# Optimization experiments

Hardware: AMD Instinct MI355X
Metric: run time of the kernel (lower is better)

Reference implementation:

```python
import jax, jax.numpy as jnp
import numpy as np
from jax import lax

V, E, H, K, B, T = 50000, 300, 512, 20, 64, 512  # vocab, embed, hidden, tags, batch, seqlen
HD = H // 2  # per-direction hidden


def setup_inputs() -> dict:
    key = jax.random.key(0)
    ks = jax.random.split(key, 12)
    s = 1.0 / np.sqrt(HD)
    inp = {
        "sentence": jax.random.randint(ks[0], (B, T), 0, V),
        "lengths": jax.random.randint(ks[1], (B,), T // 2, T + 1),
        "start_id": 18,
        "stop_id": 19,
        "embed_table": jax.random.normal(ks[2], (V, E), jnp.float32) * 0.9,
        "Wf_ih": jax.random.uniform(ks[3], (4 * HD, E), jnp.float32, -s, s),
        "Wf_hh": jax.random.uniform(ks[4], (4 * HD, HD), jnp.float32, -s, s),
        "bf": jax.random.uniform(ks[5], (4 * HD,), jnp.float32, -s, s),
        "Wb_ih": jax.random.uniform(ks[6], (4 * HD, E), jnp.float32, -s, s),
        "Wb_hh": jax.random.uniform(ks[7], (4 * HD, HD), jnp.float32, -s, s),
        "bb": jax.random.uniform(ks[8], (4 * HD,), jnp.float32, -s, s),
        "W_out": jax.random.uniform(ks[9], (K, H), jnp.float32, -s, s),
        "b_out": jax.random.uniform(ks[10], (K,), jnp.float32, -s, s),
    }
    trans = jax.random.normal(ks[11], (K, K), jnp.float32)
    trans = trans.at[18, :].set(-1000.0).at[:, 19].set(-1000.0)  # START row, STOP col
    inp["transitions"] = trans
    return inp


def _lstm(x, W_ih, W_hh, b):
    # x: [B, T, E] -> h: [B, T, HD], torch gate order i,f,g,o
    Bb = x.shape[0]
    Hd = W_hh.shape[1]
    h0 = jnp.zeros((Bb, Hd), x.dtype)

    def step(carry, xt):
        h, c = carry
        gates = xt @ W_ih.T + h @ W_hh.T + b
        i, f, g, o = jnp.split(gates, 4, axis=-1)
        c = jax.nn.sigmoid(f) * c + jax.nn.sigmoid(i) * jnp.tanh(g)
        h = jax.nn.sigmoid(o) * jnp.tanh(c)
        return (h, c), h

    _, hs = lax.scan(step, (h0, h0), x.transpose(1, 0, 2))
    return hs.transpose(1, 0, 2)


def _reverse_by_length(x, lengths):
    # reverse the valid prefix of each sequence, leaving padding in place
    t = jnp.arange(x.shape[1])[None, :]
    idx = jnp.where(t < lengths[:, None], lengths[:, None] - 1 - t, t)
    return jnp.take_along_axis(x, idx[:, :, None], axis=1)


def _emissions(sentence, lengths, embed_table, Wf_ih, Wf_hh, bf, Wb_ih, Wb_hh, bb, W_out, b_out):
    emb = embed_table[sentence]  # [B,T,E] (dropout is identity at inference)
    hf = _lstm(emb, Wf_ih, Wf_hh, bf)
    hb = _reverse_by_length(_lstm(_reverse_by_length(emb, lengths), Wb_ih, Wb_hh, bb), lengths)
    out = jnp.concatenate([hf, hb], axis=-1)  # [B,T,H]
    return out @ W_out.T + b_out  # [B,T,K]


def _viterbi(emis, lengths, transitions, stop_id):
    Bb, Tt, Kk = emis.shape
    delta0 = jnp.zeros((Bb, Kk), emis.dtype)  # faithful: init_vvars is all zeros
    valid = (jnp.arange(Tt)[None, :] < lengths[:, None]).T  # [T,B]
    ident = jnp.arange(Kk, dtype=jnp.int32)[None, :]

    def step(delta, inputs):
        emit_t, v = inputs  # [B,K], [B]
        scores = delta[:, None, :] + transitions[None, :, :]  # [B, next, prev]
        bp = jnp.argmax(scores, axis=-1).astype(jnp.int32)
        new_delta = jnp.max(scores, axis=-1) + emit_t
        delta = jnp.where(v[:, None], new_delta, delta)
        bp = jnp.where(v[:, None], bp, ident)  # pass-through at padded steps
        return delta, bp

    delta, bps = lax.scan(step, delta0, (emis.transpose(1, 0, 2), valid))
    terminal = delta + transitions[stop_id][None, :]
    best_last = jnp.argmax(terminal, axis=-1).astype(jnp.int32)  # [B]
    scores = jnp.max(terminal, axis=-1)  # [B]

    def backtrace(tag, bp_t):
        prev = jnp.take_along_axis(bp_t, tag[:, None], axis=1)[:, 0]
        return prev, prev

    _, prevs = lax.scan(backtrace, best_last, bps, reverse=True)  # [T,B]
    paths = jnp.concatenate([prevs, best_last[None, :]], axis=0).T  # [B,T+1], path[0]=START-step tag
    return scores, paths


def reference(sentence, lengths, start_id, stop_id, embed_table, Wf_ih, Wf_hh, bf,
              Wb_ih, Wb_hh, bb, W_out, b_out, transitions):
    emis = _emissions(sentence, lengths, embed_table, Wf_ih, Wf_hh, bf, Wb_ih, Wb_hh, bb, W_out, b_out)
    scores, paths = _viterbi(emis, lengths, transitions, stop_id)
    return scores, paths
```

## Files before the change

kernel.cpp:

```cpp
#include <hip/hip_runtime.h>
#include <math.h>

#define TT 512
#define BB 64
#define EE 300
#define HD 256
#define KK 20
#define NG 1024
#define RGC 8
#define RPBF 8
#define DPG 16
#define HS 260
#define LDSF (RPBF * HS)
#define LDS_FLOATS (2 * LDSF)
#define HXS 2048

__device__ __forceinline__ unsigned long long ldg_llc_u64(const unsigned long long* p) {
    return __hip_atomic_load(p, __ATOMIC_RELAXED, __HIP_MEMORY_SCOPE_AGENT);
}
__device__ __forceinline__ void stg_llc_u64(unsigned long long* p, unsigned long long v) {
    __hip_atomic_store(p, v, __ATOMIC_RELAXED, __HIP_MEMORY_SCOPE_AGENT);
}
__device__ __forceinline__ unsigned long long pack_ht(float h, int tag) {
    return ((unsigned long long)(unsigned)tag << 32) | (unsigned long long)__float_as_uint(h);
}

__global__ __launch_bounds__(256) void proj_kernel(
    const int* __restrict__ sentence, const float* __restrict__ embed,
    const float* __restrict__ Wf_ih, const float* __restrict__ bf,
    const float* __restrict__ Wb_ih, const float* __restrict__ bb,
    float* __restrict__ Pf, float* __restrict__ Pb, int t0f, int t0b)
{
    __shared__ float As[32][BB];
    __shared__ float Ws[32][64];
    const int s   = blockIdx.x;
    const int gb  = blockIdx.y;
    const int dir = gb >> 4;
    const int g0  = (gb & 15) * 64;
    const int tg  = dir ? (t0b + s) : (t0f + s);
    const int tid = threadIdx.x;
    const int tx = tid & 15, ty = tid >> 4;

    const int lrow = tid >> 2;
    const int kq   = tid & 3;
    const int word = sentence[lrow * TT + tg];
    const float* arow = embed + (size_t)word * EE;
    const float* Wih  = dir ? Wb_ih : Wf_ih;
    const float* bias = dir ? bb : bf;
    const float* wrow = Wih + (size_t)(g0 + lrow) * EE;

    float acc[4][4] = {};
    for (int k0 = 0; k0 < EE; k0 += 32) {
        __syncthreads();
        #pragma unroll
        for (int u = 0; u < 8; ++u) {
            const int k  = kq * 8 + u;
            const int kk = k0 + k;
            const bool ok = (kk < EE);
            As[k][lrow] = ok ? arow[kk] : 0.f;
            Ws[k][lrow] = ok ? wrow[kk] : 0.f;
        }
        __syncthreads();
        #pragma unroll
        for (int k = 0; k < 32; ++k) {
            const float4 a = *(const float4*)&As[k][ty * 4];
            const float4 w = *(const float4*)&Ws[k][tx * 4];
            acc[0][0] += a.x*w.x; acc[0][1] += a.x*w.y; acc[0][2] += a.x*w.z; acc[0][3] += a.x*w.w;
            acc[1][0] += a.y*w.x; acc[1][1] += a.y*w.y; acc[1][2] += a.y*w.z; acc[1][3] += a.y*w.w;
            acc[2][0] += a.z*w.x; acc[2][1] += a.z*w.y; acc[2][2] += a.z*w.z; acc[2][3] += a.z*w.w;
            acc[3][0] += a.w*w.x; acc[3][1] += a.w*w.y; acc[3][2] += a.w*w.z; acc[3][3] += a.w*w.w;
        }
    }
    float* Pd = (dir ? Pb : Pf) + (size_t)s * BB * NG;
    const float4 bv = *(const float4*)&bias[g0 + tx * 4];
    #pragma unroll
    for (int i = 0; i < 4; ++i) {
        float4 v;
        v.x = acc[i][0] + bv.x; v.y = acc[i][1] + bv.y;
        v.z = acc[i][2] + bv.z; v.w = acc[i][3] + bv.w;
        *(float4*)(Pd + (size_t)(ty * 4 + i) * NG + g0 + tx * 4) = v;
    }
}

__device__ __forceinline__ void gemv8(const float* __restrict__ base,
                                      const float4 (&wr)[4][4], int s,
                                      float res[4])
{
    float acc[4][8];
    #pragma unroll
    for (int g = 0; g < 4; ++g)
        #pragma unroll
        for (int r = 0; r < 8; ++r) acc[g][r] = 0.f;

    #pragma unroll
    for (int r = 0; r < 8; ++r) {
        const float* hr = base + r * HS + 4 * s;
        const float4 h0 = *(const float4*)(hr + 0);
        const float4 h1 = *(const float4*)(hr + 64);
        const float4 h2 = *(const float4*)(hr + 128);
        const float4 h3 = *(const float4*)(hr + 192);
        #pragma unroll
        for (int g = 0; g < 4; ++g) {
            float a4 = acc[g][r];
            a4 = fmaf(wr[g][0].x, h0.x, a4); a4 = fmaf(wr[g][0].y, h0.y, a4);
            a4 = fmaf(wr[g][0].z, h0.z, a4); a4 = fmaf(wr[g][0].w, h0.w, a4);
            a4 = fmaf(wr[g][1].x, h1.x, a4); a4 = fmaf(wr[g][1].y, h1.y, a4);
            a4 = fmaf(wr[g][1].z, h1.z, a4); a4 = fmaf(wr[g][1].w, h1.w, a4);
            a4 = fmaf(wr[g][2].x, h2.x, a4); a4 = fmaf(wr[g][2].y, h2.y, a4);
            a4 = fmaf(wr[g][2].z, h2.z, a4); a4 = fmaf(wr[g][2].w, h2.w, a4);
            a4 = fmaf(wr[g][3].x, h3.x, a4); a4 = fmaf(wr[g][3].y, h3.y, a4);
            a4 = fmaf(wr[g][3].z, h3.z, a4); a4 = fmaf(wr[g][3].w, h3.w, a4);
            acc[g][r] = a4;
        }
    }
    float r1[4][4];
    #pragma unroll
    for (int g = 0; g < 4; ++g)
        #pragma unroll
        for (int m = 0; m < 4; ++m) {
            const float sendv = (s & 1) ? acc[g][2*m]   : acc[g][2*m+1];
            const float keepv = (s & 1) ? acc[g][2*m+1] : acc[g][2*m];
            r1[g][m] = keepv + __shfl_xor(sendv, 1);
        }
    float r2[4][2];
    #pragma unroll
    for (int g = 0; g < 4; ++g)
        #pragma unroll
        for (int m = 0; m < 2; ++m) {
            const float sendv = (s & 2) ? r1[g][2*m]   : r1[g][2*m+1];
            const float keepv = (s & 2) ? r1[g][2*m+1] : r1[g][2*m];
            r2[g][m] = keepv + __shfl_xor(sendv, 2);
        }
    #pragma unroll
    for (int g = 0; g < 4; ++g) {
        const float sendv = (s & 4) ? r2[g][0] : r2[g][1];
        const float keepv = (s & 4) ? r2[g][1] : r2[g][0];
        const float r3 = keepv + __shfl_xor(sendv, 4);
        res[g] = r3 + __shfl_xor(r3, 8);
    }
}

__global__ __launch_bounds__(256, 1) void lstm_kernel(
    const float* __restrict__ Pf, const float* __restrict__ Pb,
    const float* __restrict__ Wf_hh, const float* __restrict__ Wb_hh,
    const int* __restrict__ lengths,
    float* __restrict__ HF, float* __restrict__ HB,
    unsigned long long* __restrict__ hx2,
    float* __restrict__ cbuf,
    int step0, int nsteps)
{
    __shared__ float lds[LDS_FLOATS];
    const int blk  = blockIdx.x;
    const int rg   = blk & 7;
    const int j    = blk >> 3;
    const int tid  = threadIdx.x;
    const int w    = tid >> 6;
    const int lane = tid & 63;
    const int d    = lane >> 4;
    const int s    = lane & 15;
    const int rs   = s & 7;
    const int dg   = j * DPG + w * 4 + d;
    const int grow = rg * RPBF + rs;
    const int kk   = tid >> 3, rr = tid & 7;

    const int len = lengths[grow];

    float4 wF[4][4], wB[4][4];
    #pragma unroll
    for (int g = 0; g < 4; ++g) {
        const float* rowF = Wf_hh + (size_t)(g * HD + dg) * HD + 4 * s;
        const float* rowB = Wb_hh + (size_t)(g * HD + dg) * HD + 4 * s;
        #pragma unroll
        for (int q = 0; q < 4; ++q) {
            wF[g][q] = *(const float4*)(rowF + 64 * q);
            wB[g][q] = *(const float4*)(rowB + 64 * q);
        }
    }

    float c_f = cbuf[((size_t)0 * HD + dg) * BB + grow];
    float c_b = cbuf[((size_t)1 * HD + dg) * BB + grow];

    unsigned long long hreg[8];
    {
        const unsigned long long* src = hx2 +
            ((size_t)(((step0 + 1) & 1) * 2 + 0) * RGC + rg) * HXS;
        #pragma unroll
        for (int it = 0; it < 8; ++it) {
            const unsigned long long* a = &src[(kk + 32 * it) * 8 + rr];
            unsigned long long v = ldg_llc_u64(a);
            while ((int)(v >> 32) != step0) v = ldg_llc_u64(a);
            hreg[it] = v;
        }
    }

    for (int u = 0; u < nsteps; ++u) {
        const int gs  = step0 + u;
        const int pbt = TT - 1 - gs;

        const float* PpF = Pf + ((size_t)u * BB + grow) * NG + dg;
        const float pfi = PpF[0], pff = PpF[256], pfg = PpF[512], pfo = PpF[768];
        const float* PpB = Pb + ((size_t)(nsteps - 1 - u) * BB + grow) * NG + dg;
        const float pbi = PpB[0], pbf = PpB[256], pbg = PpB[512], pbo = PpB[768];

        #pragma unroll
        for (int it = 0; it < 8; ++it)
            lds[rr * HS + kk + 32 * it] =
                __uint_as_float((unsigned)(hreg[it] & 0xffffffffull));
        __syncthreads();
        const unsigned long long* srcB = hx2 +
            ((size_t)(((gs + 1) & 1) * 2 + 1) * RGC + rg) * HXS;
        #pragma unroll
        for (int it = 0; it < 8; ++it)
            hreg[it] = ldg_llc_u64(&srcB[(kk + 32 * it) * 8 + rr]);

        float res[4];
        gemv8(lds, wF, s, res);

        #pragma unroll
        for (int it = 0; it < 8; ++it) {
            unsigned long long v = hreg[it];
            if ((int)(v >> 32) != gs) {
                const unsigned long long* a = &srcB[(kk + 32 * it) * 8 + rr];
                do { v = ldg_llc_u64(a); } while ((int)(v >> 32) != gs);
            }
            hreg[it] = v;
        }

        const float igf = 1.f / (1.f + expf(-(res[0] + pfi)));
        const float fgf = 1.f / (1.f + expf(-(res[1] + pff)));
        const float ogf = 1.f / (1.f + expf(-(res[3] + pfo)));
        const float gtf = tanhf(res[2] + pfg);
        c_f = fgf * c_f + igf * gtf;
        const float hnf = ogf * tanhf(c_f);
        if (s < 8) {
            stg_llc_u64(&hx2[((size_t)((gs & 1) * 2 + 0) * RGC + rg) * HXS
                             + (size_t)dg * 8 + rs], pack_ht(hnf, gs + 1));
            HF[((size_t)gs * HD + dg) * BB + grow] = hnf;
        }

        #pragma unroll
        for (int it = 0; it < 8; ++it)
            lds[LDSF + rr * HS + kk + 32 * it] =
                __uint_as_float((unsigned)(hreg[it] & 0xffffffffull));
        __syncthreads();
        const unsigned long long* srcF = hx2 +
            ((size_t)((gs & 1) * 2 + 0) * RGC + rg) * HXS;
        #pragma unroll
        for (int it = 0; it < 8; ++it)
            hreg[it] = ldg_llc_u64(&srcF[(kk + 32 * it) * 8 + rr]);

        gemv8(lds + LDSF, wB, s, res);

        #pragma unroll
        for (int it = 0; it < 8; ++it) {
            unsigned long long v = hreg[it];
            if ((int)(v >> 32) != gs + 1) {
                const unsigned long long* a = &srcF[(kk + 32 * it) * 8 + rr];
                do { v = ldg_llc_u64(a); } while ((int)(v >> 32) != gs + 1);
            }
            hreg[it] = v;
        }

        const float igb = 1.f / (1.f + expf(-(res[0] + pbi)));
        const float fgb = 1.f / (1.f + expf(-(res[1] + pbf)));
        const float ogb = 1.f / (1.f + expf(-(res[3] + pbo)));
        const float gtb = tanhf(res[2] + pbg);
        const float cnb = fgb * c_b + igb * gtb;
        float hnb = ogb * tanhf(cnb);
        const bool vOK = (pbt < len);
        c_b = vOK ? cnb : c_b;
        hnb = vOK ? hnb : 0.f;
        if (s < 8) {
            stg_llc_u64(&hx2[((size_t)((gs & 1) * 2 + 1) * RGC + rg) * HXS
                             + (size_t)dg * 8 + rs], pack_ht(hnb, gs + 1));
            HB[((size_t)pbt * HD + dg) * BB + grow] = hnb;
        }
    }

    if (s < 8) {
        cbuf[((size_t)0 * HD + dg) * BB + grow] = c_f;
        cbuf[((size_t)1 * HD + dg) * BB + grow] = c_b;
    }
}

__global__ __launch_bounds__(256) void emis_kernel(
    const float* __restrict__ HF, const float* __restrict__ HB,
    const float* __restrict__ W_out, const float* __restrict__ b_out,
    float* __restrict__ emis)
{
    const int t = blockIdx.x;
    const int b = threadIdx.x & 63;
    int jg = threadIdx.x >> 6;
    jg = __builtin_amdgcn_readfirstlane(jg);

    float acc[5];
    #pragma unroll
    for (int u = 0; u < 5; ++u) acc[u] = b_out[jg + 4 * u];

    const float* hf = HF + (size_t)t * HD * BB + b;
    const float* hb = HB + (size_t)t * HD * BB + b;
    for (int k = 0; k < HD; ++k) {
        const float hv = hf[(size_t)k * BB];
        #pragma unroll
        for (int u = 0; u < 5; ++u)
            acc[u] = fmaf(hv, W_out[(size_t)(jg + 4 * u) * 512 + k], acc[u]);
    }
    for (int k = 0; k < HD; ++k) {
        const float hv = hb[(size_t)k * BB];
        #pragma unroll
        for (int u = 0; u < 5; ++u)
            acc[u] = fmaf(hv, W_out[(size_t)(jg + 4 * u) * 512 + HD + k], acc[u]);
    }
    #pragma unroll
    for (int u = 0; u < 5; ++u)
        emis[((size_t)t * BB + b) * KK + jg + 4 * u] = acc[u];
}

__global__ __launch_bounds__(64) void viterbi_kernel(
    const float* __restrict__ emis, const int* __restrict__ lengths,
    const float* __restrict__ trans, const int* __restrict__ stop_id_p,
    float* __restrict__ out)
{
    __shared__ float tr[KK * KK];
    __shared__ float delta[KK], nd[KK];
    __shared__ unsigned char bp[TT][KK];
    const int b = blockIdx.x;
    const int tid = threadIdx.x;
    for (int i = tid; i < KK * KK; i += 64) tr[i] = trans[i];
    if (tid < KK) delta[tid] = 0.f;
    const int len = lengths[b];
    __syncthreads();

    for (int t = 0; t < TT; ++t) {
        if (tid < KK) {
            if (t < len) {
                float best = delta[0] + tr[tid * KK + 0];
                int am = 0;
                for (int p2 = 1; p2 < KK; ++p2) {
                    const float v = delta[p2] + tr[tid * KK + p2];
                    if (v > best) { best = v; am = p2; }
                }
                nd[tid] = best + emis[((size_t)t * BB + b) * KK + tid];
                bp[t][tid] = (unsigned char)am;
            } else {
                nd[tid] = delta[tid];
                bp[t][tid] = (unsigned char)tid;
            }
        }
        __syncthreads();
        if (tid < KK) delta[tid] = nd[tid];
        __syncthreads();
    }

    if (tid == 0) {
        const int stop_id = *stop_id_p;
        float best = delta[0] + tr[stop_id * KK + 0];
        int bl = 0;
        for (int jx = 1; jx < KK; ++jx) {
            const float v = delta[jx] + tr[stop_id * KK + jx];
            if (v > best) { best = v; bl = jx; }
        }
        out[b] = best;
        float* pout = out + BB + (size_t)b * (TT + 1);
        pout[TT] = (float)bl;
        int tag = bl;
        for (int t = TT - 1; t >= 0; --t) {
            tag = bp[t][tag];
            pout[t] = (float)tag;
        }
    }
}

extern "C" void kernel_launch(void* const* d_in, const int* in_sizes, int n_in,
                              void* d_out, int out_size, void* d_ws, size_t ws_size,
                              hipStream_t stream) {
    const int*   sentence = (const int*)d_in[0];
    const int*   lengths  = (const int*)d_in[1];
    const int*   stop_id  = (const int*)d_in[3];
    const float* embed    = (const float*)d_in[4];
    const float* Wf_ih    = (const float*)d_in[5];
    const float* Wf_hh    = (const float*)d_in[6];
    const float* bf       = (const float*)d_in[7];
    const float* Wb_ih    = (const float*)d_in[8];
    const float* Wb_hh    = (const float*)d_in[9];
    const float* bb       = (const float*)d_in[10];
    const float* W_out    = (const float*)d_in[11];
    const float* b_out    = (const float*)d_in[12];
    const float* trans    = (const float*)d_in[13];
    float* out = (float*)d_out;

    const size_t hf_elems   = (size_t)TT * HD * BB;
    const size_t emis_elems = (size_t)TT * BB * KK;
    const size_t hx_u64     = (size_t)2 * 2 * RGC * HD * RPBF;
    const size_t cbuf_elems = (size_t)2 * HD * BB;
    const size_t fixed_bytes = (2 * hf_elems + emis_elems + cbuf_elems) * 4 + hx_u64 * 8;

    int CH = 0;
    const int cands[6] = {256, 128, 64, 32, 16, 8};
    for (int i = 0; i < 6; ++i) {
        const size_t need = fixed_bytes + 2ull * cands[i] * BB * NG * 4;
        if (need <= ws_size) { CH = cands[i]; break; }
    }
    if (CH == 0) return;

    float* Pf    = (float*)d_ws;
    float* Pb    = Pf + (size_t)CH * BB * NG;
    float* HF    = Pb + (size_t)CH * BB * NG;
    float* HB    = HF + hf_elems;
    float* emis  = HB + hf_elems;
    unsigned long long* hx2 = (unsigned long long*)(emis + emis_elems);
    float* cbuf  = (float*)(hx2 + hx_u64);

    hipMemsetAsync(hx2, 0, hx_u64 * 8 + cbuf_elems * 4, stream);

    const int nch = TT / CH;
    for (int c = 0; c < nch; ++c) {
        const int t0f = c * CH;
        const int t0b = TT - (c + 1) * CH;
        proj_kernel<<<dim3(CH, 32), 256, 0, stream>>>(
            sentence, embed, Wf_ih, bf, Wb_ih, bb, Pf, Pb, t0f, t0b);
        lstm_kernel<<<dim3(128), 256, 0, stream>>>(
            Pf, Pb, Wf_hh, Wb_hh, lengths, HF, HB, hx2, cbuf, c * CH, CH);
    }
    emis_kernel<<<dim3(TT), 256, 0, stream>>>(HF, HB, W_out, b_out, emis);
    viterbi_kernel<<<dim3(BB), 64, 0, stream>>>(emis, lengths, trans, stop_id, out);
}
```

Measured before the change: 4.411 ms.

## Split forward/backward LSTM directions across waves and double grid to 256 blocks

The persistent LSTM kernel used to run both directions sequentially inside each block, with two barrier/poll phases per step. Now waves 0-1 handle the forward direction and waves 2-3 the backward direction, each over 8 hidden units, and the grid doubles to 256 blocks. Both directions' hidden states are polled and staged together once per step. This halves per-thread weight registers and the serial critical path per step. The cost is more blocks taking part in the spin-wait cross-block sync, and a dependence on all 256 blocks being co-resident, which the persistent design needs.

```diff
diff --git a/kernel.cpp b/kernel.cpp
--- a/kernel.cpp
+++ b/kernel.cpp
@@ -9,7 +9,6 @@
 #define NG 1024
 #define RGC 8
 #define RPBF 8
-#define DPG 16
 #define HS 260
 #define LDSF (RPBF * HS)
 #define LDS_FLOATS (2 * LDSF)
@@ -152,135 +151,131 @@
     __shared__ float lds[LDS_FLOATS];
     const int blk  = blockIdx.x;
     const int rg   = blk & 7;
-    const int j    = blk >> 3;
+    const int jg   = blk >> 3;
     const int tid  = threadIdx.x;
     const int w    = tid >> 6;
+    const int dirw = w >> 1;
+    const int wh   = w & 1;
     const int lane = tid & 63;
     const int d    = lane >> 4;
     const int s    = lane & 15;
     const int rs   = s & 7;
-    const int dg   = j * DPG + w * 4 + d;
+    const int dg   = jg * 8 + wh * 4 + d;
     const int grow = rg * RPBF + rs;
-    const int kk   = tid >> 3, rr = tid & 7;
-
-    const int len = lengths[grow];
-
-    float4 wF[4][4], wB[4][4];
+    const int kb   = tid >> 3;
+    const int rr   = tid & 7;
+
+    const float* Whh = dirw ? Wb_hh : Wf_hh;
+    const float* P   = dirw ? Pb : Pf;
+    float* Hout      = dirw ? HB : HF;
+    const int len    = lengths[grow];
+
+    float4 wR[4][4];
     #pragma unroll
     for (int g = 0; g < 4; ++g) {
-        const float* rowF = Wf_hh + (size_t)(g * HD + dg) * HD + 4 * s;
-        const float* rowB = Wb_hh + (size_t)(g * HD + dg) * HD + 4 * s;
-        #pragma unroll
-        for (int q = 0; q < 4; ++q) {
-            wF[g][q] = *(const float4*)(rowF + 64 * q);
-            wB[g][q] = *(const float4*)(rowB + 64 * q);
-        }
-    }
-
-    float c_f = cbuf[((size_t)0 * HD + dg) * BB + grow];
-    float c_b = cbuf[((size_t)1 * HD + dg) * BB + grow];
-
-    unsigned long long hreg[8];
+        const float* wrow = Whh + (size_t)(g * HD + dg) * HD + 4 * s;
+        #pragma unroll
+        for (int q = 0; q < 4; ++q)
+            wR[g][q] = *(const float4*)(wrow + 64 * q);
+    }
+
+    float c0 = cbuf[((size_t)dirw * HD + dg) * BB + grow];
+
+    unsigned long long hF[8], hB[8];
     {
-        const unsigned long long* src = hx2 +
-            ((size_t)(((step0 + 1) & 1) * 2 + 0) * RGC + rg) * HXS;
+        const unsigned long long* s0F = hx2 + ((size_t)(((step0 + 1) & 1) * 2 + 0) * RGC + rg) * HXS;
+        const unsigned long long* s0B = hx2 + ((size_t)(((step0 + 1) & 1) * 2 + 1) * RGC + rg) * HXS;
         #pragma unroll
         for (int it = 0; it < 8; ++it) {
-            const unsigned long long* a = &src[(kk + 32 * it) * 8 + rr];
-            unsigned long long v = ldg_llc_u64(a);
-            while ((int)(v >> 32) != step0) v = ldg_llc_u64(a);
-            hreg[it] = v;
+            hF[it] = ldg_llc_u64(&s0F[(kb + 32 * it) * 8 + rr]);
+            hB[it] = ldg_llc_u64(&s0B[(kb + 32 * it) * 8 + rr]);
+        }
+        #pragma unroll
+        for (int it = 0; it < 8; ++it) {
+            unsigned long long v = hF[it];
+            if ((int)(v >> 32) != step0) {
+                const unsigned long long* a = &s0F[(kb + 32 * it) * 8 + rr];
+                do { v = ldg_llc_u64(a); } while ((int)(v >> 32) != step0);
+            }
+            hF[it] = v;
+            v = hB[it];
+            if ((int)(v >> 32) != step0) {
+                const unsigned long long* a = &s0B[(kb + 32 * it) * 8 + rr];
+                do { v = ldg_llc_u64(a); } while ((int)(v >> 32) != step0);
+            }
+            hB[it] = v;
         }
     }
 
     for (int u = 0; u < nsteps; ++u) {
-        const int gs  = step0 + u;
-        const int pbt = TT - 1 - gs;
-
-        const float* PpF = Pf + ((size_t)u * BB + grow) * NG + dg;
-        const float pfi = PpF[0], pff = PpF[256], pfg = PpF[512], pfo = PpF[768];
-        const float* PpB = Pb + ((size_t)(nsteps - 1 - u) * BB + grow) * NG + dg;
-        const float pbi = PpB[0], pbf = PpB[256], pbg = PpB[512], pbo = PpB[768];
-
-        #pragma unroll
-        for (int it = 0; it < 8; ++it)
-            lds[rr * HS + kk + 32 * it] =
-                __uint_as_float((unsigned)(hreg[it] & 0xffffffffull));
-        __syncthreads();
-        const unsigned long long* srcB = hx2 +
-            ((size_t)(((gs + 1) & 1) * 2 + 1) * RGC + rg) * HXS;
-        #pragma unroll
-        for (int it = 0; it < 8; ++it)
-            hreg[it] = ldg_llc_u64(&srcB[(kk + 32 * it) * 8 + rr]);
+        const int gs   = step0 + u;
+        const int pbt  = TT - 1 - gs;
+        const int p    = dirw ? pbt : gs;
+        const int slot = dirw ? (nsteps - 1 - u) : u;
+
+        const float* Pp = P + ((size_t)slot * BB + grow) * NG + dg;
+        const float pi = Pp[0], pf = Pp[256], pg = Pp[512], po = Pp[768];
+
+        #pragma unroll
+        for (int it = 0; it < 8; ++it) {
+            lds[rr * HS + kb + 32 * it] =
+                __uint_as_float((unsigned)(hF[it] & 0xffffffffull));
+            lds[LDSF + rr * HS + kb + 32 * it] =
+                __uint_as_float((unsigned)(hB[it] & 0xffffffffull));
+        }
+        __syncthreads();
 
         float res[4];
-        gemv8(lds, wF, s, res);
-
-        #pragma unroll
-        for (int it = 0; it < 8; ++it) {
-            unsigned long long v = hreg[it];
-            if ((int)(v >> 32) != gs) {
-                const unsigned long long* a = &srcB[(kk + 32 * it) * 8 + rr];
-                do { v = ldg_llc_u64(a); } while ((int)(v >> 32) != gs);
+        gemv8(dirw ? (lds + LDSF) : lds, wR, s, res);
+
+        const float ig = 1.f / (1.f + expf(-(res[0] + pi)));
+        const float fg = 1.f / (1.f + expf(-(res[1] + pf)));
+        const float og = 1.f / (1.f + expf(-(res[3] + po)));
+        const float gt = tanhf(res[2] + pg);
+        float cn = fg * c0 + ig * gt;
+        float hn = og * tanhf(cn);
+        if (dirw) {
+            const bool v0 = (pbt < len);
+            c0 = v0 ? cn : c0;  hn = v0 ? hn : 0.f;
+        } else {
+            c0 = cn;
+        }
+
+        if (s < 8) {
+            stg_llc_u64(&hx2[((size_t)((gs & 1) * 2 + dirw) * RGC + rg) * HXS
+                             + (size_t)dg * 8 + rs], pack_ht(hn, gs + 1));
+            Hout[((size_t)p * HD + dg) * BB + grow] = hn;
+        }
+
+        if (u + 1 < nsteps) {
+            const unsigned long long* sF = hx2 + ((size_t)((gs & 1) * 2 + 0) * RGC + rg) * HXS;
+            const unsigned long long* sB = hx2 + ((size_t)((gs & 1) * 2 + 1) * RGC + rg) * HXS;
+            #pragma unroll
+            for (int it = 0; it < 8; ++it) {
+                hF[it] = ldg_llc_u64(&sF[(kb + 32 * it) * 8 + rr]);
+                hB[it] = ldg_llc_u64(&sB[(kb + 32 * it) * 8 + rr]);
             }
-            hreg[it] = v;
-        }
-
-        const float igf = 1.f / (1.f + expf(-(res[0] + pfi)));
-        const float fgf = 1.f / (1.f + expf(-(res[1] + pff)));
-        const float ogf = 1.f / (1.f + expf(-(res[3] + pfo)));
-        const float gtf = tanhf(res[2] + pfg);
-        c_f = fgf * c_f + igf * gtf;
-        const float hnf = ogf * tanhf(c_f);
-        if (s < 8) {
-            stg_llc_u64(&hx2[((size_t)((gs & 1) * 2 + 0) * RGC + rg) * HXS
-                             + (size_t)dg * 8 + rs], pack_ht(hnf, gs + 1));
-            HF[((size_t)gs * HD + dg) * BB + grow] = hnf;
-        }
-
-        #pragma unroll
-        for (int it = 0; it < 8; ++it)
-            lds[LDSF + rr * HS + kk + 32 * it] =
-                __uint_as_float((unsigned)(hreg[it] & 0xffffffffull));
-        __syncthreads();
-        const unsigned long long* srcF = hx2 +
-            ((size_t)((gs & 1) * 2 + 0) * RGC + rg) * HXS;
-        #pragma unroll
-        for (int it = 0; it < 8; ++it)
-            hreg[it] = ldg_llc_u64(&srcF[(kk + 32 * it) * 8 + rr]);
-
-        gemv8(lds + LDSF, wB, s, res);
-
-        #pragma unroll
-        for (int it = 0; it < 8; ++it) {
-            unsigned long long v = hreg[it];
-            if ((int)(v >> 32) != gs + 1) {
-                const unsigned long long* a = &srcF[(kk + 32 * it) * 8 + rr];
-                do { v = ldg_llc_u64(a); } while ((int)(v >> 32) != gs + 1);
+            #pragma unroll
+            for (int it = 0; it < 8; ++it) {
+                unsigned long long v = hF[it];
+                if ((int)(v >> 32) != gs + 1) {
+                    const unsigned long long* a = &sF[(kb + 32 * it) * 8 + rr];
+                    do { v = ldg_llc_u64(a); } while ((int)(v >> 32) != gs + 1);
+                }
+                hF[it] = v;
+                v = hB[it];
+                if ((int)(v >> 32) != gs + 1) {
+                    const unsigned long long* a = &sB[(kb + 32 * it) * 8 + rr];
+                    do { v = ldg_llc_u64(a); } while ((int)(v >> 32) != gs + 1);
+                }
+                hB[it] = v;
             }
-            hreg[it] = v;
-        }
-
-        const float igb = 1.f / (1.f + expf(-(res[0] + pbi)));
-        const float fgb = 1.f / (1.f + expf(-(res[1] + pbf)));
-        const float ogb = 1.f / (1.f + expf(-(res[3] + pbo)));
-        const float gtb = tanhf(res[2] + pbg);
-        const float cnb = fgb * c_b + igb * gtb;
-        float hnb = ogb * tanhf(cnb);
-        const bool vOK = (pbt < len);
-        c_b = vOK ? cnb : c_b;
-        hnb = vOK ? hnb : 0.f;
-        if (s < 8) {
-            stg_llc_u64(&hx2[((size_t)((gs & 1) * 2 + 1) * RGC + rg) * HXS
-                             + (size_t)dg * 8 + rs], pack_ht(hnb, gs + 1));
-            HB[((size_t)pbt * HD + dg) * BB + grow] = hnb;
-        }
-    }
-
-    if (s < 8) {
-        cbuf[((size_t)0 * HD + dg) * BB + grow] = c_f;
-        cbuf[((size_t)1 * HD + dg) * BB + grow] = c_b;
-    }
+        }
+        __syncthreads();
+    }
+
+    if (s < 8)
+        cbuf[((size_t)dirw * HD + dg) * BB + grow] = c0;
 }
 
 __global__ __launch_bounds__(256) void emis_kernel(
@@ -419,7 +414,7 @@
         const int t0b = TT - (c + 1) * CH;
         proj_kernel<<<dim3(CH, 32), 256, 0, stream>>>(
             sentence, embed, Wf_ih, bf, Wb_ih, bb, Pf, Pb, t0f, t0b);
-        lstm_kernel<<<dim3(128), 256, 0, stream>>>(
+        lstm_kernel<<<dim3(256), 256, 0, stream>>>(
             Pf, Pb, Wf_hh, Wb_hh, lengths, HF, HB, hx2, cbuf, c * CH, CH);
     }
     emis_kernel<<<dim3(TT), 256, 0, stream>>>(HF, HB, W_out, b_out, emis);
```

Result: faster. 3.858 ms (-12.5%).
